# Optimization experiments

Hardware: AMD Instinct MI355X
Metric: run time of the kernel (lower is better)

## Reference

```python
import jax, jax.numpy as jnp
import numpy as np

N_EDGES = 1_250_000
N_NODES = 100_000
EDGE_DIM = 64
N_RADIAL = 16
OUT_DIM = 1


def setup_inputs() -> dict:
    key = jax.random.key(0)
    ks = jax.random.split(key, 12)
    s_e = 1.0 / np.sqrt(EDGE_DIM)
    s_r = 1.0 / np.sqrt(N_RADIAL)
    return {
        "x": jax.random.normal(ks[0], (N_EDGES, EDGE_DIM), jnp.float32),
        "rbf": jax.random.uniform(ks[1], (N_EDGES, N_RADIAL), jnp.float32),
        "idx_i": jax.random.randint(ks[2], (N_EDGES,), 0, N_NODES, jnp.int64),
        "num_nodes": N_NODES,
        # rbf_dense: Dense(n_radial, edge_dim, bias=False) -> weight (edge_dim, n_radial)
        "W_rbf": jax.random.normal(ks[3], (EDGE_DIM, N_RADIAL), jnp.float32) * s_r,
        # three hidden Dense(edge_dim, edge_dim) with bias
        "W1": jax.random.normal(ks[4], (EDGE_DIM, EDGE_DIM), jnp.float32) * s_e,
        "b1": jnp.zeros((EDGE_DIM,), jnp.float32),
        "W2": jax.random.normal(ks[5], (EDGE_DIM, EDGE_DIM), jnp.float32) * s_e,
        "b2": jnp.zeros((EDGE_DIM,), jnp.float32),
        "W3": jax.random.normal(ks[6], (EDGE_DIM, EDGE_DIM), jnp.float32) * s_e,
        "b3": jnp.zeros((EDGE_DIM,), jnp.float32),
        # final Dense(edge_dim, out_dim, bias=False) -> weight (out_dim, edge_dim)
        "W_out": jax.random.normal(ks[7], (OUT_DIM, EDGE_DIM), jnp.float32) * s_e,
    }


def swish(h):
    # Swish(beta=1.0): h * sigmoid(h)
    return h * jax.nn.sigmoid(h)


def reference(x, rbf, idx_i, num_nodes, W_rbf, W1, b1, W2, b2, W3, b3, W_out):
    # edge gating: Dense(rbf) * x  -> (n_edge, edge_dim)
    e = (rbf @ W_rbf.T) * x
    # scatter-add edges to center nodes -> (n_node, edge_dim)
    h = jax.ops.segment_sum(e, idx_i, num_segments=num_nodes)
    h = swish(h @ W1.T + b1)
    h = swish(h @ W2.T + b2)
    h = swish(h @ W3.T + b3)
    return h @ W_out.T
```

## Files before the change

### kernel.cpp

```cpp
#include <hip/hip_runtime.h>
#include <hip/hip_bf16.h>
#include <cstdint>


__global__ __launch_bounds__(256) void edge_kernel(
    const float* __restrict__ x,
    const float* __restrict__ rbf,
    const int*   __restrict__ idx,
    const float* __restrict__ Wrbf,
    float* __restrict__ hacc,
    int n_edges, int n_nodes)
{
    const int lane   = threadIdx.x & 63;
    const int wave   = blockIdx.x * (blockDim.x >> 6) + (threadIdx.x >> 6);
    const int nwaves = gridDim.x * (blockDim.x >> 6);

    float w[16];
    {
        const float4* wp = (const float4*)(Wrbf + (size_t)lane * 16);
        float4 a = wp[0], b = wp[1], c = wp[2], d = wp[3];
        w[0]=a.x; w[1]=a.y; w[2]=a.z; w[3]=a.w;
        w[4]=b.x; w[5]=b.y; w[6]=b.z; w[7]=b.w;
        w[8]=c.x; w[9]=c.y; w[10]=c.z; w[11]=c.w;
        w[12]=d.x; w[13]=d.y; w[14]=d.z; w[15]=d.w;
    }

    for (int e = wave; e < n_edges; e += nwaves) {
        const int node = idx[e];
        const float4* rp = (const float4*)(rbf + (size_t)e * 16);
        float4 r0 = rp[0], r1 = rp[1], r2 = rp[2], r3 = rp[3];
        float rv[16] = { r0.x, r0.y, r0.z, r0.w,
                         r1.x, r1.y, r1.z, r1.w,
                         r2.x, r2.y, r2.z, r2.w,
                         r3.x, r3.y, r3.z, r3.w };

        float g = 0.0f;
#pragma unroll
        for (int r = 0; r < 16; ++r) g = fmaf(rv[r], w[r], g);

        const float xv = x[(size_t)e * 64 + lane];
        if ((unsigned)node < (unsigned)n_nodes) {
            atomicAdd(&hacc[(size_t)node * 64 + lane], g * xv);
        }
    }
}

__device__ __forceinline__ float mlp_layer(const float* __restrict__ WT,
                                           const float* __restrict__ bias,
                                           float h, int lane)
{
    float acc = bias[lane];
#pragma unroll
    for (int k = 0; k < 64; ++k) {
        const float wk = WT[k * 64 + lane];
        const float hk = __int_as_float(
            __builtin_amdgcn_readlane(__float_as_int(h), k));
        acc = fmaf(wk, hk, acc);
    }
    return acc / (1.0f + __expf(-acc));
}

__global__ __launch_bounds__(256) void node_kernel(
    const float* __restrict__ hacc,
    const float* __restrict__ W1, const float* __restrict__ b1,
    const float* __restrict__ W2, const float* __restrict__ b2,
    const float* __restrict__ W3, const float* __restrict__ b3,
    const float* __restrict__ Wout,
    float* __restrict__ out,
    int n_nodes)
{
    __shared__ float WT[3][64 * 64];
    __shared__ float bs[3][64];
    __shared__ float wo[64];

    const int t = threadIdx.x;
    for (int i = t; i < 64 * 64; i += 256) {
        const int d = i & 63;
        const int k = i >> 6;
        WT[0][k * 64 + d] = W1[d * 64 + k];
        WT[1][k * 64 + d] = W2[d * 64 + k];
        WT[2][k * 64 + d] = W3[d * 64 + k];
    }
    if (t < 64) {
        bs[0][t] = b1[t];
        bs[1][t] = b2[t];
        bs[2][t] = b3[t];
        wo[t]    = Wout[t];
    }
    __syncthreads();

    const int lane   = t & 63;
    const int wave   = blockIdx.x * (blockDim.x >> 6) + (t >> 6);
    const int nwaves = gridDim.x * (blockDim.x >> 6);

    for (int node = wave; node < n_nodes; node += nwaves) {
        float h = hacc[(size_t)node * 64 + lane];
        h = mlp_layer(WT[0], bs[0], h, lane);
        h = mlp_layer(WT[1], bs[1], h, lane);
        h = mlp_layer(WT[2], bs[2], h, lane);

        float v = wo[lane] * h;
#pragma unroll
        for (int off = 32; off >= 1; off >>= 1) v += __shfl_xor(v, off, 64);

        if (lane == 0) out[node] = v;
    }
}

extern "C" void kernel_launch(void* const* d_in, const int* in_sizes, int n_in,
                              void* d_out, int out_size, void* d_ws, size_t ws_size,
                              hipStream_t stream)
{
    const float* x    = (const float*)d_in[0];
    const float* rbf  = (const float*)d_in[1];
    const int*   idx  = (const int*)d_in[2];
    const float* Wrbf = (const float*)d_in[4];
    const float* W1   = (const float*)d_in[5];
    const float* b1   = (const float*)d_in[6];
    const float* W2   = (const float*)d_in[7];
    const float* b2   = (const float*)d_in[8];
    const float* W3   = (const float*)d_in[9];
    const float* b3   = (const float*)d_in[10];
    const float* Wout = (const float*)d_in[11];

    const int n_edges = in_sizes[0] / 64;
    const int n_nodes = out_size;

    float* hacc = (float*)d_ws;

    hipMemsetAsync(hacc, 0, (size_t)n_nodes * 64 * sizeof(float), stream);

    edge_kernel<<<8192, 256, 0, stream>>>(x, rbf, idx, Wrbf, hacc,
                                          n_edges, n_nodes);

    node_kernel<<<2048, 256, 0, stream>>>(hacc, W1, b1, W2, b2, W3, b3, Wout,
                                          (float*)d_out, n_nodes);
}
```

Measured before the change: 854.3 us.

## Replace atomic scatter-add with CSR sort-by-node and per-node gather

Builds a CSR index over destination nodes (histogram, two-level prefix scan, scatter into a permutation), then runs one wave per node that sums its edges in registers and writes the result once, with no float atomics. This removes the 80M float atomicAdds to the node accumulator and the memset of that accumulator. In exchange it adds several small kernels, integer atomics over the edge indices, and an uncoalesced permuted gather of x and rbf rows. The old atomic path is kept as a fallback when the workspace is too small.

```diff
diff --git a/kernel.cpp b/kernel.cpp
--- a/kernel.cpp
+++ b/kernel.cpp
@@ -1,19 +1,90 @@
 #include <hip/hip_runtime.h>
-#include <hip/hip_bf16.h>
 #include <cstdint>
 
 
-__global__ __launch_bounds__(256) void edge_kernel(
+
+__global__ __launch_bounds__(256) void k_hist(
+    const int* __restrict__ idx, int* __restrict__ counts, int n_edges)
+{
+    const int i = blockIdx.x * blockDim.x + threadIdx.x;
+    const int stride = gridDim.x * blockDim.x;
+    for (int e = i; e < n_edges; e += stride)
+        atomicAdd(&counts[idx[e]], 1);
+}
+
+__global__ __launch_bounds__(256) void k_scan1(
+    const int* __restrict__ counts, int* __restrict__ offsets,
+    int* __restrict__ blocksum, int n_nodes)
+{
+    __shared__ int sh[256];
+    const int t = threadIdx.x;
+    const int i = blockIdx.x * 256 + t;
+    const int v = (i < n_nodes) ? counts[i] : 0;
+    sh[t] = v;
+    __syncthreads();
+    for (int off = 1; off < 256; off <<= 1) {
+        const int add = (t >= off) ? sh[t - off] : 0;
+        __syncthreads();
+        sh[t] += add;
+        __syncthreads();
+    }
+    if (i < n_nodes) offsets[i] = sh[t] - v;
+    if (t == 255) blocksum[blockIdx.x] = sh[255];
+}
+
+__global__ __launch_bounds__(512) void k_scan2(int* __restrict__ blocksum, int nb)
+{
+    __shared__ int sh[512];
+    const int t = threadIdx.x;
+    const int v = (t < nb) ? blocksum[t] : 0;
+    sh[t] = v;
+    __syncthreads();
+    for (int off = 1; off < 512; off <<= 1) {
+        const int add = (t >= off) ? sh[t - off] : 0;
+        __syncthreads();
+        sh[t] += add;
+        __syncthreads();
+    }
+    if (t < nb) blocksum[t] = sh[t] - v;
+}
+
+__global__ __launch_bounds__(256) void k_addbase(
+    int* __restrict__ offsets, const int* __restrict__ blocksum,
+    int* __restrict__ cursor, int n_nodes, int n_edges)
+{
+    const int i = blockIdx.x * 256 + threadIdx.x;
+    if (i < n_nodes) {
+        const int o = offsets[i] + blocksum[blockIdx.x];
+        offsets[i] = o;
+        cursor[i]  = o;
+    }
+    if (i == 0) offsets[n_nodes] = n_edges;
+}
+
+__global__ __launch_bounds__(256) void k_scatter(
+    const int* __restrict__ idx, int* __restrict__ cursor,
+    int* __restrict__ perm, int n_edges)
+{
+    const int i = blockIdx.x * blockDim.x + threadIdx.x;
+    const int stride = gridDim.x * blockDim.x;
+    for (int e = i; e < n_edges; e += stride) {
+        const int pos = atomicAdd(&cursor[idx[e]], 1);
+        perm[pos] = e;
+    }
+}
+
+__global__ __launch_bounds__(256) void k_gather(
     const float* __restrict__ x,
     const float* __restrict__ rbf,
-    const int*   __restrict__ idx,
+    const int*   __restrict__ offsets,
+    const int*   __restrict__ perm,
     const float* __restrict__ Wrbf,
     float* __restrict__ hacc,
-    int n_edges, int n_nodes)
-{
-    const int lane   = threadIdx.x & 63;
-    const int wave   = blockIdx.x * (blockDim.x >> 6) + (threadIdx.x >> 6);
-    const int nwaves = gridDim.x * (blockDim.x >> 6);
+    int n_nodes)
+{
+    const int lane = threadIdx.x & 63;
+    const int n    = blockIdx.x * (blockDim.x >> 6) + (threadIdx.x >> 6);
+    if (n >= n_nodes) return;
 
     float w[16];
     {
@@ -25,23 +96,65 @@
         w[12]=d.x; w[13]=d.y; w[14]=d.z; w[15]=d.w;
     }
 
+    const int s     = offsets[n];
+    const int e_end = offsets[n + 1];
+
+    float acc = 0.0f;
+    int e = (s < e_end) ? perm[s] : 0;
+    for (int j = s; j < e_end; ++j) {
+        const int e_nxt = (j + 1 < e_end) ? perm[j + 1] : 0;
+
+        const float4* rp = (const float4*)(rbf + (size_t)e * 16);
+        float4 r0 = rp[0], r1 = rp[1], r2 = rp[2], r3 = rp[3];
+        const float xv = x[(size_t)e * 64 + lane];
+
+        float g = 0.0f;
+        g = fmaf(r0.x, w[0],  g); g = fmaf(r0.y, w[1],  g);
+        g = fmaf(r0.z, w[2],  g); g = fmaf(r0.w, w[3],  g);
+        g = fmaf(r1.x, w[4],  g); g = fmaf(r1.y, w[5],  g);
+        g = fmaf(r1.z, w[6],  g); g = fmaf(r1.w, w[7],  g);
+        g = fmaf(r2.x, w[8],  g); g = fmaf(r2.y, w[9],  g);
+        g = fmaf(r2.z, w[10], g); g = fmaf(r2.w, w[11], g);
+        g = fmaf(r3.x, w[12], g); g = fmaf(r3.y, w[13], g);
+        g = fmaf(r3.z, w[14], g); g = fmaf(r3.w, w[15], g);
+
+        acc = fmaf(g, xv, acc);
+        e = e_nxt;
+    }
+    hacc[(size_t)n * 64 + lane] = acc;
+}
+
+__global__ __launch_bounds__(256) void edge_kernel(
+    const float* __restrict__ x, const float* __restrict__ rbf,
+    const int* __restrict__ idx, const float* __restrict__ Wrbf,
+    float* __restrict__ hacc, int n_edges, int n_nodes)
+{
+    const int lane   = threadIdx.x & 63;
+    const int wave   = blockIdx.x * (blockDim.x >> 6) + (threadIdx.x >> 6);
+    const int nwaves = gridDim.x * (blockDim.x >> 6);
+
+    float w[16];
+    {
+        const float4* wp = (const float4*)(Wrbf + (size_t)lane * 16);
+        float4 a = wp[0], b = wp[1], c = wp[2], d = wp[3];
+        w[0]=a.x; w[1]=a.y; w[2]=a.z; w[3]=a.w;
+        w[4]=b.x; w[5]=b.y; w[6]=b.z; w[7]=b.w;
+        w[8]=c.x; w[9]=c.y; w[10]=c.z; w[11]=c.w;
+        w[12]=d.x; w[13]=d.y; w[14]=d.z; w[15]=d.w;
+    }
+
     for (int e = wave; e < n_edges; e += nwaves) {
         const int node = idx[e];
         const float4* rp = (const float4*)(rbf + (size_t)e * 16);
         float4 r0 = rp[0], r1 = rp[1], r2 = rp[2], r3 = rp[3];
-        float rv[16] = { r0.x, r0.y, r0.z, r0.w,
-                         r1.x, r1.y, r1.z, r1.w,
-                         r2.x, r2.y, r2.z, r2.w,
-                         r3.x, r3.y, r3.z, r3.w };
-
+        float rv[16] = { r0.x, r0.y, r0.z, r0.w, r1.x, r1.y, r1.z, r1.w,
+                         r2.x, r2.y, r2.z, r2.w, r3.x, r3.y, r3.z, r3.w };
         float g = 0.0f;
 #pragma unroll
         for (int r = 0; r < 16; ++r) g = fmaf(rv[r], w[r], g);
-
         const float xv = x[(size_t)e * 64 + lane];
-        if ((unsigned)node < (unsigned)n_nodes) {
+        if ((unsigned)node < (unsigned)n_nodes)
             atomicAdd(&hacc[(size_t)node * 64 + lane], g * xv);
-        }
     }
 }
 
@@ -66,8 +179,7 @@
     const float* __restrict__ W2, const float* __restrict__ b2,
     const float* __restrict__ W3, const float* __restrict__ b3,
     const float* __restrict__ Wout,
-    float* __restrict__ out,
-    int n_nodes)
+    float* __restrict__ out, int n_nodes)
 {
     __shared__ float WT[3][64 * 64];
     __shared__ float bs[3][64];
@@ -82,10 +194,8 @@
         WT[2][k * 64 + d] = W3[d * 64 + k];
     }
     if (t < 64) {
-        bs[0][t] = b1[t];
-        bs[1][t] = b2[t];
-        bs[2][t] = b3[t];
-        wo[t]    = Wout[t];
+        bs[0][t] = b1[t]; bs[1][t] = b2[t]; bs[2][t] = b3[t];
+        wo[t] = Wout[t];
     }
     __syncthreads();
 
@@ -102,7 +212,6 @@
         float v = wo[lane] * h;
 #pragma unroll
         for (int off = 32; off >= 1; off >>= 1) v += __shfl_xor(v, off, 64);
-
         if (lane == 0) out[node] = v;
     }
 }
@@ -126,12 +235,36 @@
     const int n_edges = in_sizes[0] / 64;
     const int n_nodes = out_size;
 
-    float* hacc = (float*)d_ws;
-
-    hipMemsetAsync(hacc, 0, (size_t)n_nodes * 64 * sizeof(float), stream);
-
-    edge_kernel<<<8192, 256, 0, stream>>>(x, rbf, idx, Wrbf, hacc,
-                                          n_edges, n_nodes);
+    const size_t N_pad = ((size_t)n_nodes + 1 + 63) & ~(size_t)63;
+    const size_t E_pad = ((size_t)n_edges + 63) & ~(size_t)63;
+    int*   counts = (int*)d_ws;
+    int*   offs   = counts + N_pad;
+    int*   bsum   = offs + N_pad;
+    int*   perm   = bsum + 512;
+    float* hacc   = (float*)(perm + E_pad);
+
+    const size_t need = (2 * N_pad + 512 + E_pad) * sizeof(int)
+                      + (size_t)n_nodes * 64 * sizeof(float);
+
+    const int NB = (n_nodes + 255) / 256;
+
+    if (ws_size >= need && NB <= 512) {
+        hipMemsetAsync(counts, 0, (size_t)n_nodes * sizeof(int), stream);
+        k_hist   <<<2048, 256, 0, stream>>>(idx, counts, n_edges);
+        k_scan1  <<<NB,   256, 0, stream>>>(counts, offs, bsum, n_nodes);
+        k_scan2  <<<1,    512, 0, stream>>>(bsum, NB);
+        k_addbase<<<NB,   256, 0, stream>>>(offs, bsum, counts, n_nodes, n_edges);
+        k_scatter<<<2048, 256, 0, stream>>>(idx, counts, perm, n_edges);
+
+        const int gblocks = (n_nodes + 3) / 4;
+        k_gather<<<gblocks, 256, 0, stream>>>(x, rbf, offs, perm, Wrbf,
+                                              hacc, n_nodes);
+    } else {
+        hacc = (float*)d_ws;
+        hipMemsetAsync(hacc, 0, (size_t)n_nodes * 64 * sizeof(float), stream);
+        edge_kernel<<<8192, 256, 0, stream>>>(x, rbf, idx, Wrbf, hacc,
+                                              n_edges, n_nodes);
+    }
 
     node_kernel<<<2048, 256, 0, stream>>>(hacc, W1, b1, W2, b2, W3, b3, Wout,
                                           (float*)d_out, n_nodes);
```

Result: slower. 956.7 us (+12.0%).
